# Performance work log

Hardware: AMD Instinct MI355X
Metric: run time of the kernel (lower is better)

## Reference

```python
import jax, jax.numpy as jnp
import numpy as np


def setup_inputs() -> dict:
    key = jax.random.key(0)
    k1, k2 = jax.random.split(key)
    N_SYMBOLS, D = 256, 512
    B, T = 256, 1024
    # uniform init like the torch module: U(-val, val), val = sqrt(3)*sqrt(2/(N+D))
    val = np.sqrt(3.0) * np.sqrt(2.0 / (N_SYMBOLS + D))
    weight = jax.random.uniform(k1, (N_SYMBOLS, D), jnp.float32, -val, val)
    x = jax.random.randint(k2, (B, T), 0, N_SYMBOLS, dtype=jnp.int64)
    end_ids = jnp.arange(2, dtype=jnp.int64)  # end_symbols_ids = [0, 1]
    return {"weight": weight, "x": x, "end_ids": end_ids}


def reference(weight, x, end_ids):
    # embedding gather: [B, T, D]
    emb = weight[x]
    # pre-scaled end-symbol vectors (vec = end_vectors[_id] * 1.5): [E, D]
    end_vecs = weight[end_ids] * jnp.asarray(1.5, weight.dtype)
    B, T, D = emb.shape

    def step(carry, inp):
        vec, has = carry          # vec: [B, D], has: [B] bool ("vec is not None")
        e_t, x_t = inp            # e_t: [B, D], x_t: [B]
        eq = x_t[:, None] == end_ids[None, :]   # [B, E]
        is_end = eq.any(axis=1)                 # token is an end symbol
        idx = jnp.argmax(eq, axis=1)            # which end symbol
        # at end positions: update vec, skip the add (the `continue`)
        out = e_t + jnp.where((has & ~is_end)[:, None], vec, jnp.zeros((), e_t.dtype))
        new_vec = jnp.where(is_end[:, None], end_vecs[idx], vec)
        new_has = has | is_end
        return (new_vec, new_has), out

    init = (jnp.zeros((B, D), emb.dtype), jnp.zeros((B,), dtype=bool))
    _, outs = jax.lax.scan(
        step, init, (emb.transpose(1, 0, 2), x.T), reverse=True
    )  # outs: [T, B, D] in original time order
    return outs.transpose(1, 0, 2)
```

## Files before the change

### kernel.cpp

```cpp
#include <hip/hip_runtime.h>


typedef float f4 __attribute__((ext_vector_type(4)));

constexpr int TT = 1024;
constexpr int DD = 512;
constexpr int C4 = DD / 4;
constexpr int SPLIT = 8;
constexpr int NW = TT / 64;

__global__ __launch_bounds__(1024) void embeder_kernel(
    const float* __restrict__ weight,
    const int* __restrict__ x,
    const int* __restrict__ end_ids,
    float* __restrict__ out)
{
    __shared__ int wmin[NW];
    __shared__ int code[TT];

    const int b    = blockIdx.x / SPLIT;
    const int sp   = blockIdx.x % SPLIT;
    const int tid  = threadIdx.x;
    const int wid  = tid >> 6;
    const int lane = tid & 63;
    const int e0 = end_ids[0], e1 = end_ids[1];
    const int INF = 0x7FFFFFFF;

    const int c4 = tid & 127;
    const f4* wv = (const f4*)weight;
    f4 ea = wv[e0 * C4 + c4] * 1.5f;
    f4 eb = wv[e1 * C4 + c4] * 1.5f;

    int sym = x[b * TT + tid];
    bool is_end = (sym == e0) || (sym == e1);
    int v = is_end ? ((tid << 1) | (sym == e0 ? 0 : 1)) : INF;

    #pragma unroll
    for (int off = 1; off < 64; off <<= 1) {
        int u = __shfl_down(v, off);
        v = (lane + off < 64) ? min(v, u) : v;
    }
    if (lane == 0) wmin[wid] = v;
    __syncthreads();

    int tailMin = INF;
    for (int w = wid + 1; w < NW; ++w) tailMin = min(tailMin, wmin[w]);

    int nvWave = __shfl_down(v, 1);
    int nv = (lane < 63) ? min(nvWave, tailMin) : tailMin;

    int sel = 0;
    if (!is_end && nv != INF) sel = (nv & 1) + 1;
    code[tid] = sym | (sel << 16);
    __syncthreads();

    f4* ov = (f4*)out + (size_t)b * TT * C4;

    const int iters = (TT * C4) / 1024 / SPLIT;
    const int kbase = sp * iters;
    #pragma unroll
    for (int k = 0; k < iters; ++k) {
        int idx = tid + (kbase + k) * 1024;
        int t   = idx >> 7;
        int c    = code[t];
        int symt = c & 0xFFFF;
        int selt = c >> 16;
        f4 wq = wv[symt * C4 + c4];
        if (selt) {
            f4 e = (selt == 1) ? ea : eb;
            wq += e;
        }
        __builtin_nontemporal_store(wq, &ov[idx]);
    }
}

extern "C" void kernel_launch(void* const* d_in, const int* in_sizes, int n_in,
                              void* d_out, int out_size, void* d_ws, size_t ws_size,
                              hipStream_t stream) {
    const float* weight  = (const float*)d_in[0];
    const int*   x       = (const int*)d_in[1];
    const int*   end_ids = (const int*)d_in[2];
    float*       out     = (float*)d_out;

    const int B = in_sizes[1] / TT;
    embeder_kernel<<<B * SPLIT, 1024, 0, stream>>>(weight, x, end_ids, out);
}
```

Baseline: 97.74 us.

## Split into code-precompute kernel and grid-stride streaming gather kernel

Moves the per-row end-symbol scan into a separate kernel that writes packed codes to workspace, then runs a persistent grid-stride streaming kernel with 256-thread blocks over the whole output. The aim is to stop the big 1024-thread blocks from redoing the scan eight times each and to improve occupancy and store streaming. The cost is an extra kernel launch, a workspace round trip, and global reads of codes in place of shared memory reads.

```diff
diff --git a/kernel.cpp b/kernel.cpp
--- a/kernel.cpp
+++ b/kernel.cpp
@@ -6,30 +6,20 @@
 constexpr int TT = 1024;
 constexpr int DD = 512;
 constexpr int C4 = DD / 4;
-constexpr int SPLIT = 8;
 constexpr int NW = TT / 64;
 
-__global__ __launch_bounds__(1024) void embeder_kernel(
-    const float* __restrict__ weight,
+__global__ __launch_bounds__(1024) void codes_kernel(
     const int* __restrict__ x,
     const int* __restrict__ end_ids,
-    float* __restrict__ out)
+    int* __restrict__ codes)
 {
     __shared__ int wmin[NW];
-    __shared__ int code[TT];
-
-    const int b    = blockIdx.x / SPLIT;
-    const int sp   = blockIdx.x % SPLIT;
+    const int b    = blockIdx.x;
     const int tid  = threadIdx.x;
     const int wid  = tid >> 6;
     const int lane = tid & 63;
     const int e0 = end_ids[0], e1 = end_ids[1];
     const int INF = 0x7FFFFFFF;
-
-    const int c4 = tid & 127;
-    const f4* wv = (const f4*)weight;
-    f4 ea = wv[e0 * C4 + c4] * 1.5f;
-    f4 eb = wv[e1 * C4 + c4] * 1.5f;
 
     int sym = x[b * TT + tid];
     bool is_end = (sym == e0) || (sym == e1);
@@ -51,18 +41,36 @@
 
     int sel = 0;
     if (!is_end && nv != INF) sel = (nv & 1) + 1;
-    code[tid] = sym | (sel << 16);
-    __syncthreads();
+    codes[b * TT + tid] = sym | (sel << 16);
+}
 
-    f4* ov = (f4*)out + (size_t)b * TT * C4;
+constexpr int BLK  = 256;
+constexpr int GRID = 2048;
+constexpr int NTH  = BLK * GRID;
 
-    const int iters = (TT * C4) / 1024 / SPLIT;
-    const int kbase = sp * iters;
-    #pragma unroll
-    for (int k = 0; k < iters; ++k) {
-        int idx = tid + (kbase + k) * 1024;
+__global__ __launch_bounds__(BLK) void stream_kernel(
+    const float* __restrict__ weight,
+    const int* __restrict__ codes,
+    const int* __restrict__ end_ids,
+    float* __restrict__ out,
+    int total_c4)
+{
+    const int tid  = threadIdx.x;
+    const int base = blockIdx.x * BLK + tid;
+    const int c4   = base & 127;
+    const int e0 = end_ids[0], e1 = end_ids[1];
+
+    const f4* wv = (const f4*)weight;
+    f4 ea = wv[e0 * C4 + c4] * 1.5f;
+    f4 eb = wv[e1 * C4 + c4] * 1.5f;
+    f4* ov = (f4*)out;
+
+    const int iters = total_c4 / NTH;
+    #pragma unroll 8
+    for (int i = 0; i < iters; ++i) {
+        int idx = base + i * NTH;
         int t   = idx >> 7;
-        int c    = code[t];
+        int c   = codes[t];
         int symt = c & 0xFFFF;
         int selt = c >> 16;
         f4 wq = wv[symt * C4 + c4];
@@ -81,7 +89,10 @@
     const int*   x       = (const int*)d_in[1];
     const int*   end_ids = (const int*)d_in[2];
     float*       out     = (float*)d_out;
+    int*         codes   = (int*)d_ws;
 
     const int B = in_sizes[1] / TT;
-    embeder_kernel<<<B * SPLIT, 1024, 0, stream>>>(weight, x, end_ids, out);
+    codes_kernel<<<B, 1024, 0, stream>>>(x, end_ids, codes);
+    const int total_c4 = B * TT * C4;
+    stream_kernel<<<GRID, BLK, 0, stream>>>(weight, codes, end_ids, out, total_c4);
 }
```

After: 132.5 us. 1.36x slower.
